# Kernel tuning notes

Hardware: AMD Instinct MI355X
Metric: run time of the kernel (lower is better)

## Reference

```python
import jax, jax.numpy as jnp
import numpy as np
import math

N_EMBED = 1024
N_HEAD = 16
BLOCK_SIZE = 2048

def setup_inputs() -> dict:
    key = jax.random.key(0)
    k1, k2, k3, k4, k5 = jax.random.split(key, 5)
    s = 0.02
    x = jax.random.normal(k1, (2, 2048, N_EMBED), dtype=jnp.float32)
    W_qkv = jax.random.normal(k2, (N_EMBED, 3 * N_EMBED), dtype=jnp.float32) * s
    b_qkv = jax.random.normal(k3, (3 * N_EMBED,), dtype=jnp.float32) * s
    W_out = jax.random.normal(k4, (N_EMBED, N_EMBED), dtype=jnp.float32) * s
    b_out = jax.random.normal(k5, (N_EMBED,), dtype=jnp.float32) * s
    return {"x": x, "W_qkv": W_qkv, "b_qkv": b_qkv, "W_out": W_out, "b_out": b_out}

def reference(x, W_qkv, b_qkv, W_out, b_out):
    b, s, d = x.shape
    hd = d // N_HEAD  # head dim
    qkv = x @ W_qkv + b_qkv                       # [b, s, 3d]
    q, k, v = jnp.split(qkv, 3, axis=-1)
    # [b, h, s, hd]
    q = q.reshape(b, s, N_HEAD, hd).transpose(0, 2, 1, 3)
    k = k.reshape(b, s, N_HEAD, hd).transpose(0, 2, 1, 3)
    v = v.reshape(b, s, N_HEAD, hd).transpose(0, 2, 1, 3)
    scale = 1.0 / math.sqrt(hd)
    sims = jnp.einsum('bhqd,bhkd->bhqk', q, k) * scale  # [b, h, s, s]
    causal = jnp.tril(jnp.ones((s, s), dtype=bool))
    sims = jnp.where(causal[None, None], sims, -jnp.inf)
    probs = jax.nn.softmax(sims, axis=-1)
    attn = jnp.einsum('bhqk,bhkd->bhqd', probs, v)       # [b, h, s, hd]
    attn = attn.transpose(0, 2, 1, 3).reshape(b, s, d)
    return attn @ W_out + b_out
```

## Files before the change

### kernel.cpp

```cpp
#include <hip/hip_runtime.h>
#include <hip/hip_bf16.h>

typedef __attribute__((ext_vector_type(8))) short short8;
typedef __attribute__((ext_vector_type(4))) short short4v;
typedef __attribute__((ext_vector_type(4))) float f32x4;
typedef __attribute__((ext_vector_type(16))) float f32x16;
typedef __attribute__((ext_vector_type(4))) unsigned int u32x4;
typedef unsigned short u16;

__device__ __forceinline__ u16 f2bf(float f) {
  __hip_bfloat16 h = __float2bfloat16(f);
  return __builtin_bit_cast(unsigned short, h);
}

__device__ __forceinline__ unsigned pack2(float lo, float hi) {
  return (unsigned)f2bf(lo) | ((unsigned)f2bf(hi) << 16);
}

__device__ __forceinline__ void gload16(const u16* g, u16* l) {
  __builtin_amdgcn_global_load_lds(
      (const __attribute__((address_space(1))) unsigned int*)g,
      (__attribute__((address_space(3))) unsigned int*)l, 16, 0, 0);
}

__global__ void cvt_x_kernel(const float* __restrict__ in, u16* __restrict__ out, int n) {
  int i = (blockIdx.x * blockDim.x + threadIdx.x) * 4;
  if (i >= n) return;
  float4 f = *(const float4*)(in + i);
  uint2 pk;
  pk.x = pack2(f.x, f.y);
  pk.y = pack2(f.z, f.w);
  *(uint2*)(out + i) = pk;
}

__global__ void tcvt_kernel(const float* __restrict__ in, u16* __restrict__ out, int N) {
  __shared__ float tile[32][33];
  int n0 = blockIdx.x * 32, k0 = blockIdx.y * 32;
  int tx = threadIdx.x, ty = threadIdx.y;
#pragma unroll
  for (int r = 0; r < 4; ++r) {
    int k = ty + r * 8;
    tile[k][tx] = in[(size_t)(k0 + k) * N + n0 + tx];
  }
  __syncthreads();
#pragma unroll
  for (int r = 0; r < 4; ++r) {
    int n = ty + r * 8;
    out[(size_t)(n0 + n) * 1024 + k0 + tx] = f2bf(tile[tx][n]);
  }
}

template <int EPI>
__global__ __launch_bounds__(256, 2) void gemm_kernel(const u16* __restrict__ A,
                                                      const u16* __restrict__ Bt,
                                                      const float* __restrict__ bias,
                                                      void* __restrict__ outp) {
  __shared__ u16 Al[128 * 64];
  __shared__ u16 Bl[128 * 64];
  const int tid = threadIdx.x;
  const int lane = tid & 63, wid = tid >> 6;
  const int l15 = lane & 15, lg = lane >> 4;
  const int wm = wid >> 1, wn = wid & 1;
  const int m0 = blockIdx.y * 128, n0 = blockIdx.x * 128;

  f32x4 acc[4][4] = {};

  for (int k0 = 0; k0 < 1024; k0 += 64) {
    __syncthreads();
#pragma unroll
    for (int i = 0; i < 4; ++i) {
      int p = i * 4096 + tid * 16;
      int row = p >> 7;
      int lslot = ((p >> 4) & 7) ^ (row & 7);
      gload16(A + (size_t)(m0 + row) * 1024 + k0 + lslot * 8, Al + i * 2048 + wid * 512);
      gload16(Bt + (size_t)(n0 + row) * 1024 + k0 + lslot * 8, Bl + i * 2048 + wid * 512);
    }
    __syncthreads();
#pragma unroll
    for (int ks = 0; ks < 2; ++ks) {
      short8 af[4], bfr[4];
#pragma unroll
      for (int m = 0; m < 4; ++m) {
        int row = wm * 64 + m * 16 + l15;
        af[m] = *(const short8*)((const char*)Al + row * 128 + (((ks * 4 + lg) ^ (row & 7)) << 4));
      }
#pragma unroll
      for (int n = 0; n < 4; ++n) {
        int row = wn * 64 + n * 16 + l15;
        bfr[n] = *(const short8*)((const char*)Bl + row * 128 + (((ks * 4 + lg) ^ (row & 7)) << 4));
      }
#pragma unroll
      for (int m = 0; m < 4; ++m)
#pragma unroll
        for (int n = 0; n < 4; ++n)
          acc[m][n] = __builtin_amdgcn_mfma_f32_16x16x32_bf16(af[m], bfr[n], acc[m][n], 0, 0, 0);
    }
  }

  if (EPI == 0) {
    u16* qkv = (u16*)outp;
#pragma unroll
    for (int m = 0; m < 4; ++m)
#pragma unroll
      for (int n = 0; n < 4; ++n) {
        const int gcol = n0 + wn * 64 + n * 16 + l15;
        const int which = gcol >> 10, dd = gcol & 1023;
        const int h = dd >> 6, hd = dd & 63;
        const float bb = bias[gcol];
        const int grow0 = m0 + wm * 64 + m * 16 + lg * 4;
        const int b = grow0 >> 11, s0 = grow0 & 2047;
        if (which == 2) {
          short4v pk;
#pragma unroll
          for (int j = 0; j < 4; ++j) pk[j] = (short)f2bf(acc[m][n][j] + bb);
          *(short4v*)(qkv + (size_t)2 * 4194304 + ((size_t)(b * 16 + h) * 64 + hd) * 2048 + s0) = pk;
        } else {
          const float sc = (which == 0) ? 0.18033688011112042f : 1.0f;
#pragma unroll
          for (int j = 0; j < 4; ++j) {
            float v = (acc[m][n][j] + bb) * sc;
            qkv[(size_t)which * 4194304 + ((size_t)(b * 16 + h) * 2048 + s0 + j) * 64 + hd] = f2bf(v);
          }
        }
      }
  } else {
    float* O = (float*)outp;
#pragma unroll
    for (int m = 0; m < 4; ++m)
#pragma unroll
      for (int n = 0; n < 4; ++n) {
        const int gcol = n0 + wn * 64 + n * 16 + l15;
        const float bb = bias[gcol];
#pragma unroll
        for (int j = 0; j < 4; ++j) {
          const int grow = m0 + wm * 64 + m * 16 + lg * 4 + j;
          O[(size_t)grow * 1024 + gcol] = acc[m][n][j] + bb;
        }
      }
  }
}

__global__ __launch_bounds__(256, 2) void attn_kernel(const u16* __restrict__ Q,
                                                      const u16* __restrict__ K,
                                                      const u16* __restrict__ VT,
                                                      u16* __restrict__ Aout) {
  const int bh = blockIdx.y;
  const int p = blockIdx.x;
  const int tid = threadIdx.x, lane = tid & 63, wid = tid >> 6;
  const int l31 = lane & 31, h = lane >> 5;
  const int qs = wid & 1, kp = wid >> 1;

  __shared__ __align__(16) char smem[36864];
  u16(*Kl)[4096] = (u16(*)[4096])smem;
  u16(*Vl)[4096] = (u16(*)[4096])(smem + 16384);

  const u16* Qb = Q + (size_t)bh * 2048 * 64;
  const u16* Kb = K + (size_t)bh * 2048 * 64;
  const u16* Vb = VT + (size_t)bh * 64 * 2048;

  const int qA = p * 64 + qs * 32;
  const int qB = (31 - p) * 64 + qs * 32;
  const int R = 32 - p;

  short8 qfA[4], qfB[4];
#pragma unroll
  for (int ks = 0; ks < 4; ++ks) {
    qfA[ks] = *(const short8*)(Qb + (size_t)(qA + l31) * 64 + ks * 16 + h * 8);
    qfB[ks] = *(const short8*)(Qb + (size_t)(qB + l31) * 64 + ks * 16 + h * 8);
  }

  f32x16 accA[2] = {}, accB[2] = {};
  float mA = -1e30f, mB = -1e30f, lA = 0.f, lB = 0.f;

  auto stage = [&](int buf, size_t kb) {
#pragma unroll
    for (int i = 0; i < 2; ++i) {
      const int row = i * 32 + (tid >> 3);
      const int sc = ((tid & 7) ^ (row & 7)) * 8;
      gload16(Kb + (kb + row) * 64 + sc, &Kl[buf][i * 2048 + wid * 512]);
      gload16(Vb + (size_t)row * 2048 + kb + sc, &Vl[buf][i * 2048 + wid * 512]);
    }
  };

  stage(0, 0);
  __syncthreads();

  for (int t = 0; t < R; ++t) {
    const int cur = t & 1;
    if (t + 1 < R) stage(cur ^ 1, (size_t)(t + 1) * 64);

    const int kvbase = t * 64 + kp * 32;
    const bool actB = kvbase <= qB + 31;
    const bool actA = kvbase <= qA + 31;
    if (actB) {
      short8 kf[4], vf[2][2];
      const int krow = kp * 32 + l31;
#pragma unroll
      for (int ks = 0; ks < 4; ++ks)
        kf[ks] = *(const short8*)((const char*)&Kl[cur][0] + krow * 128 +
                                  (((ks * 2 + h) ^ (krow & 7)) << 4));
#pragma unroll
      for (int n = 0; n < 2; ++n)
#pragma unroll
        for (int ks = 0; ks < 2; ++ks) {
          const int row = n * 32 + l31;
          vf[n][ks] = *(const short8*)((const char*)&Vl[cur][0] + row * 128 +
                                       (((kp * 4 + ks * 2 + h) ^ (row & 7)) << 4));
        }

      auto strip = [&](const short8(&qf)[4], f32x16(&acc)[2], float& m, float& l, int q0) {
        f32x16 sa = {};
#pragma unroll
        for (int ks = 0; ks < 4; ++ks)
          sa = __builtin_amdgcn_mfma_f32_32x32x16_bf16(kf[ks], qf[ks], sa, 0, 0, 0);
        if (kvbase == q0) {
#pragma unroll
          for (int r = 0; r < 16; ++r) {
            const int kvr = (r & 3) + 8 * (r >> 2) + 4 * h;
            if (kvr > l31) sa[r] = -1e30f;
          }
        }
        float rm = fmaxf(fmaxf(fmaxf(sa[0], sa[1]), fmaxf(sa[2], sa[3])),
                         fmaxf(fmaxf(sa[4], sa[5]), fmaxf(sa[6], sa[7])));
        rm = fmaxf(rm, fmaxf(fmaxf(fmaxf(sa[8], sa[9]), fmaxf(sa[10], sa[11])),
                             fmaxf(fmaxf(sa[12], sa[13]), fmaxf(sa[14], sa[15]))));
        rm = fmaxf(rm, __shfl_xor(rm, 32));
        if (!__all(rm <= m + 5.0f)) {
          const float mn = fmaxf(m, rm);
          const float corr = exp2f(m - mn);
          m = mn;
          l *= corr;
#pragma unroll
          for (int n = 0; n < 2; ++n)
#pragma unroll
            for (int r = 0; r < 16; ++r) acc[n][r] *= corr;
        }
#pragma unroll
        for (int r = 0; r < 16; ++r) sa[r] = exp2f(sa[r] - m);
        float rs = (((sa[0] + sa[1]) + (sa[2] + sa[3])) + ((sa[4] + sa[5]) + (sa[6] + sa[7]))) +
                   (((sa[8] + sa[9]) + (sa[10] + sa[11])) + ((sa[12] + sa[13]) + (sa[14] + sa[15])));
        l += rs + __shfl_xor(rs, 32);
        unsigned c[8], s[8];
#pragma unroll
        for (int i = 0; i < 8; ++i) c[i] = pack2(sa[2 * i], sa[2 * i + 1]);
#pragma unroll
        for (int i = 0; i < 8; ++i) s[i] = __shfl_xor(c[i], 32);
        u32x4 w0, w1;
        if (h == 0) {
          w0 = (u32x4){c[0], c[1], s[0], s[1]};
          w1 = (u32x4){c[4], c[5], s[4], s[5]};
        } else {
          w0 = (u32x4){s[2], s[3], c[2], c[3]};
          w1 = (u32x4){s[6], s[7], c[6], c[7]};
        }
        const short8 pk0 = __builtin_bit_cast(short8, w0);
        const short8 pk1 = __builtin_bit_cast(short8, w1);
#pragma unroll
        for (int n = 0; n < 2; ++n) {
          acc[n] = __builtin_amdgcn_mfma_f32_32x32x16_bf16(vf[n][0], pk0, acc[n], 0, 0, 0);
          acc[n] = __builtin_amdgcn_mfma_f32_32x32x16_bf16(vf[n][1], pk1, acc[n], 0, 0, 0);
        }
      };

      strip(qfB, accB, mB, lB, qB);
      if (actA) strip(qfA, accA, mA, lA, qA);
    }
    __syncthreads();
  }

  float* comb = (float*)smem;
  float* pA = comb + ((qs * 2 + 0) * 64 + lane) * 36;
  float* pB = comb + ((qs * 2 + 1) * 64 + lane) * 36;
  if (kp == 1) {
    pA[0] = mA; pA[1] = lA;
    pB[0] = mB; pB[1] = lB;
#pragma unroll
    for (int n = 0; n < 2; ++n)
#pragma unroll
      for (int r = 0; r < 16; ++r) {
        pA[2 + n * 16 + r] = accA[n][r];
        pB[2 + n * 16 + r] = accB[n][r];
      }
  }
  __syncthreads();
  if (kp == 0) {
    const int b = bh >> 4, hh = bh & 15;
    auto merge_store = [&](const float* pp, const f32x16(&acc)[2], float m0, float l0, int q0) {
      const float m1 = pp[0], l1 = pp[1];
      const float mn = fmaxf(m0, m1);
      const float c0 = exp2f(m0 - mn), c1 = exp2f(m1 - mn);
      const float inv = 1.0f / (l0 * c0 + l1 * c1);
      u16* rowp = Aout + (size_t)(b * 2048 + q0 + l31) * 1024 + hh * 64;
#pragma unroll
      for (int n = 0; n < 2; ++n)
#pragma unroll
        for (int r = 0; r < 16; r += 2) {
          const int hd = n * 32 + (r & 3) + 8 * (r >> 2) + 4 * h;
          const float v0 = (acc[n][r] * c0 + pp[2 + n * 16 + r] * c1) * inv;
          const float v1 = (acc[n][r + 1] * c0 + pp[2 + n * 16 + r + 1] * c1) * inv;
          *(unsigned*)(rowp + hd) = pack2(v0, v1);
        }
    };
    merge_store(pA, accA, mA, lA, qA);
    merge_store(pB, accB, mB, lB, qB);
  }
}

extern "C" void kernel_launch(void* const* d_in, const int* in_sizes, int n_in,
                              void* d_out, int out_size, void* d_ws, size_t ws_size,
                              hipStream_t stream) {
  const float* x = (const float*)d_in[0];
  const float* Wqkv = (const float*)d_in[1];
  const float* bqkv = (const float*)d_in[2];
  const float* Wout = (const float*)d_in[3];
  const float* bout = (const float*)d_in[4];

  char* ws = (char*)d_ws;
  u16* Xb = (u16*)(ws + 0);
  u16* WqkvT = (u16*)(ws + 8388608);
  u16* WoutT = (u16*)(ws + 14680064);
  u16* QKV = (u16*)(ws + 16777216);
  u16* Attn = Xb;

  cvt_x_kernel<<<4096, 256, 0, stream>>>(x, Xb, 4194304);
  tcvt_kernel<<<dim3(96, 32), dim3(32, 8), 0, stream>>>(Wqkv, WqkvT, 3072);
  tcvt_kernel<<<dim3(32, 32), dim3(32, 8), 0, stream>>>(Wout, WoutT, 1024);
  gemm_kernel<0><<<dim3(24, 32), 256, 0, stream>>>(Xb, WqkvT, bqkv, QKV);
  attn_kernel<<<dim3(16, 32), 256, 0, stream>>>(QKV, QKV + 4194304, QKV + 8388608, Attn);
  gemm_kernel<1><<<dim3(8, 32), 256, 0, stream>>>(Attn, WoutT, bout, d_out);
}
```

Before: 113.0 us.

## Remap V fragment loads to skip cross-lane P shuffles, add MFMA priority hints

The V operand is now loaded from LDS as two 8-byte halves whose k-ordering matches the per-lane layout of the softmax probabilities. The P operand can then be packed directly from each lane's own registers, which removes eight cross-lane shuffles and a select per strip. It also wraps the MFMA groups in s_setprio to favour matrix issue across waves, and rebalances the row-max reduction tree. In exchange it doubles the number of LDS read instructions for V and may add bank conflicts from the smaller reads.

```diff
diff --git a/kernel.cpp b/kernel.cpp
--- a/kernel.cpp
+++ b/kernel.cpp
@@ -193,26 +193,35 @@
     const bool actB = kvbase <= qB + 31;
     const bool actA = kvbase <= qA + 31;
     if (actB) {
-      short8 kf[4], vf[2][2];
+      short8 kf[4];
       const int krow = kp * 32 + l31;
 #pragma unroll
       for (int ks = 0; ks < 4; ++ks)
         kf[ks] = *(const short8*)((const char*)&Kl[cur][0] + krow * 128 +
                                   (((ks * 2 + h) ^ (krow & 7)) << 4));
-#pragma unroll
-      for (int n = 0; n < 2; ++n)
+      short8 vf[2][2];
+#pragma unroll
+      for (int n = 0; n < 2; ++n) {
+        const int row = n * 32 + l31;
+        const int rx = row & 7;
+        const char* base = (const char*)&Vl[cur][0] + row * 128;
 #pragma unroll
         for (int ks = 0; ks < 2; ++ks) {
-          const int row = n * 32 + l31;
-          vf[n][ks] = *(const short8*)((const char*)&Vl[cur][0] + row * 128 +
-                                       (((kp * 4 + ks * 2 + h) ^ (row & 7)) << 4));
-        }
+          const int cb = kp * 32 + ks * 16 + 4 * h;
+          const int c2 = cb + 8;
+          const short4v lo = *(const short4v*)(base + (((cb >> 3) ^ rx) << 4) + ((cb & 4) << 1));
+          const short4v hi = *(const short4v*)(base + (((c2 >> 3) ^ rx) << 4) + ((c2 & 4) << 1));
+          vf[n][ks] = (short8){lo[0], lo[1], lo[2], lo[3], hi[0], hi[1], hi[2], hi[3]};
+        }
+      }
 
       auto strip = [&](const short8(&qf)[4], f32x16(&acc)[2], float& m, float& l, int q0) {
         f32x16 sa = {};
+        __builtin_amdgcn_s_setprio(1);
 #pragma unroll
         for (int ks = 0; ks < 4; ++ks)
           sa = __builtin_amdgcn_mfma_f32_32x32x16_bf16(kf[ks], qf[ks], sa, 0, 0, 0);
+        __builtin_amdgcn_s_setprio(0);
         if (kvbase == q0) {
 #pragma unroll
           for (int r = 0; r < 16; ++r) {
@@ -220,10 +229,12 @@
             if (kvr > l31) sa[r] = -1e30f;
           }
         }
-        float rm = fmaxf(fmaxf(fmaxf(sa[0], sa[1]), fmaxf(sa[2], sa[3])),
-                         fmaxf(fmaxf(sa[4], sa[5]), fmaxf(sa[6], sa[7])));
-        rm = fmaxf(rm, fmaxf(fmaxf(fmaxf(sa[8], sa[9]), fmaxf(sa[10], sa[11])),
-                             fmaxf(fmaxf(sa[12], sa[13]), fmaxf(sa[14], sa[15]))));
+        const float t0 = fmaxf(fmaxf(sa[0], sa[1]), sa[2]);
+        const float t1 = fmaxf(fmaxf(sa[3], sa[4]), sa[5]);
+        const float t2 = fmaxf(fmaxf(sa[6], sa[7]), sa[8]);
+        const float t3 = fmaxf(fmaxf(sa[9], sa[10]), sa[11]);
+        const float t4 = fmaxf(fmaxf(sa[12], sa[13]), sa[14]);
+        float rm = fmaxf(fmaxf(fmaxf(t0, t1), t2), fmaxf(fmaxf(t3, t4), sa[15]));
         rm = fmaxf(rm, __shfl_xor(rm, 32));
         if (!__all(rm <= m + 5.0f)) {
           const float mn = fmaxf(m, rm);
@@ -240,26 +251,18 @@
         float rs = (((sa[0] + sa[1]) + (sa[2] + sa[3])) + ((sa[4] + sa[5]) + (sa[6] + sa[7]))) +
                    (((sa[8] + sa[9]) + (sa[10] + sa[11])) + ((sa[12] + sa[13]) + (sa[14] + sa[15])));
         l += rs + __shfl_xor(rs, 32);
-        unsigned c[8], s[8];
+        unsigned c[8];
 #pragma unroll
         for (int i = 0; i < 8; ++i) c[i] = pack2(sa[2 * i], sa[2 * i + 1]);
-#pragma unroll
-        for (int i = 0; i < 8; ++i) s[i] = __shfl_xor(c[i], 32);
-        u32x4 w0, w1;
-        if (h == 0) {
-          w0 = (u32x4){c[0], c[1], s[0], s[1]};
-          w1 = (u32x4){c[4], c[5], s[4], s[5]};
-        } else {
-          w0 = (u32x4){s[2], s[3], c[2], c[3]};
-          w1 = (u32x4){s[6], s[7], c[6], c[7]};
-        }
-        const short8 pk0 = __builtin_bit_cast(short8, w0);
-        const short8 pk1 = __builtin_bit_cast(short8, w1);
+        const short8 pk0 = __builtin_bit_cast(short8, (u32x4){c[0], c[1], c[2], c[3]});
+        const short8 pk1 = __builtin_bit_cast(short8, (u32x4){c[4], c[5], c[6], c[7]});
+        __builtin_amdgcn_s_setprio(1);
 #pragma unroll
         for (int n = 0; n < 2; ++n) {
           acc[n] = __builtin_amdgcn_mfma_f32_32x32x16_bf16(vf[n][0], pk0, acc[n], 0, 0, 0);
           acc[n] = __builtin_amdgcn_mfma_f32_32x32x16_bf16(vf[n][1], pk1, acc[n], 0, 0, 0);
         }
+        __builtin_amdgcn_s_setprio(0);
       };
 
       strip(qfB, accB, mB, lB, qB);
```

Result: no change. 112.2 us (-0.7%).
